# Kernel tuning notes

Measured on AMD Instinct MI355X. Metric: run time of the kernel, lower is better.

The kernel has to match this reference:

```python
import jax, jax.numpy as jnp
import numpy as np

B, T, I, U, O, BB = 256, 1024, 64, 256, 64, 128  # batch, seq, input, units, output, backbone_units

def lecun_tanh(x):
    return 1.7159 * jnp.tanh(0.666 * x)

def setup_inputs() -> dict:
    key = jax.random.key(0)
    ks = jax.random.split(key, 13)
    def lin(k, fan_in, fan_out):
        bound = 1.0 / np.sqrt(fan_in)
        kw, kb = jax.random.split(k)
        W = jax.random.uniform(kw, (fan_in, fan_out), jnp.float32, -bound, bound)
        b = jax.random.uniform(kb, (fan_out,), jnp.float32, -bound, bound)
        return W, b
    x = jax.random.normal(ks[0], (B, T, I), jnp.float32)
    W_bb, b_bb = lin(ks[1], I + U, BB)   # backbone Linear
    W_ff1, b_ff1 = lin(ks[2], BB, U)
    W_ff2, b_ff2 = lin(ks[3], BB, U)
    W_ta, b_ta = lin(ks[4], BB, U)       # time_a
    W_tb, b_tb = lin(ks[5], BB, U)       # time_b
    W_fc, b_fc = lin(ks[6], U, O)        # readout
    return {"x": x, "W_bb": W_bb, "b_bb": b_bb, "W_ff1": W_ff1, "b_ff1": b_ff1,
            "W_ff2": W_ff2, "b_ff2": b_ff2, "W_ta": W_ta, "b_ta": b_ta,
            "W_tb": W_tb, "b_tb": b_tb, "W_fc": W_fc, "b_fc": b_fc}

def reference(x, W_bb, b_bb, W_ff1, b_ff1, W_ff2, b_ff2, W_ta, b_ta, W_tb, b_tb, W_fc, b_fc):
    ts = jnp.float32(1.0)  # default elapsed time per step
    def step(h, xt):
        z = jnp.concatenate([xt, h], axis=-1)          # [B, I+U]
        g = lecun_tanh(z @ W_bb + b_bb)                # [B, BB]
        ff1 = jnp.tanh(g @ W_ff1 + b_ff1)              # [B, U]
        ff2 = jnp.tanh(g @ W_ff2 + b_ff2)
        t_interp = jax.nn.sigmoid((g @ W_ta + b_ta) * ts + (g @ W_tb + b_tb))
        h_new = ff1 * (1.0 - t_interp) + t_interp * ff2
        return h_new, h_new
    h0 = jnp.zeros((x.shape[0], U), x.dtype)
    h_last, hs = jax.lax.scan(step, h0, jnp.swapaxes(x, 0, 1))  # hs: [T, B, U]
    hs = jnp.swapaxes(hs, 0, 1)                                  # [B, T, U]
    out = hs @ W_fc + b_fc                                       # [B, T, O]
    return out, h_last
```

## Files before the change

### kernel.cpp

```cpp
#include <hip/hip_runtime.h>
#include <stdint.h>

#define B_ 256
#define T_ 1024
#define I_ 64
#define U_ 256
#define O_ 64
#define BB_ 128

typedef unsigned int u32;
typedef unsigned short u16;
typedef _Float16 half2_t __attribute__((ext_vector_type(2)));
typedef _Float16 f16x8 __attribute__((ext_vector_type(8)));
typedef float f32x4 __attribute__((ext_vector_type(4)));

#if defined(__has_builtin)
#if __has_builtin(__builtin_amdgcn_fdot2)
#define USE_DOT2 1
#else
#define USE_DOT2 0
#endif
#else
#define USE_DOT2 0
#endif

static __device__ __forceinline__ u32 packpair(float a, float b) {
  half2_t h; h.x = (_Float16)a; h.y = (_Float16)b;
  return __builtin_bit_cast(u32, h);
}
static __device__ __forceinline__ float unpack_lo(u32 u) {
  half2_t h = __builtin_bit_cast(half2_t, u); return (float)h.x;
}
static __device__ __forceinline__ float unpack_hi(u32 u) {
  half2_t h = __builtin_bit_cast(half2_t, u); return (float)h.y;
}
static __device__ __forceinline__ float dot2acc(u32 w, u32 z, float acc) {
#if USE_DOT2
  return __builtin_amdgcn_fdot2(__builtin_bit_cast(half2_t, w),
                                __builtin_bit_cast(half2_t, z), acc, false);
#else
  half2_t hw = __builtin_bit_cast(half2_t, w);
  half2_t hz = __builtin_bit_cast(half2_t, z);
  acc += (float)hw.x * (float)hz.x;
  acc += (float)hw.y * (float)hz.y;
  return acc;
#endif
}

template <int CTRL>
static __device__ __forceinline__ float dpp_mov_f(float v) {
  return __builtin_bit_cast(float, __builtin_amdgcn_update_dpp(
      0, __builtin_bit_cast(int, v), CTRL, 0xF, 0xF, true));
}
#define DPP_XOR1 0xB1
#define DPP_XOR2 0x4E
#define DPP_HMIR 0x141
#define DPP_MIRR 0x140

static __device__ __forceinline__ float fast_tanh(float x) {
  return 1.0f - 2.0f / (1.0f + __expf(2.0f * x));
}
static __device__ __forceinline__ float fast_sigmoid(float x) {
  return 1.0f / (1.0f + __expf(-x));
}

static __device__ __forceinline__ float rcpf(float x) {
#if defined(__has_builtin) && __has_builtin(__builtin_amdgcn_rcpf)
  return __builtin_amdgcn_rcpf(x);
#else
  return 1.0f / x;
#endif
}
static __device__ __forceinline__ float exp2fast(float x) {
#if defined(__has_builtin) && __has_builtin(__builtin_amdgcn_exp2f)
  return __builtin_amdgcn_exp2f(x);
#else
  return exp2f(x);
#endif
}

static __device__ __forceinline__ f32x4 mfma16(uint4 a, uint4 b, f32x4 c) {
  return __builtin_amdgcn_mfma_f32_16x16x32_f16(
      __builtin_bit_cast(f16x8, a), __builtin_bit_cast(f16x8, b), c, 0, 0, 0);
}

#define LOG2E 1.44269504f

__global__ __launch_bounds__(512, 2)
void px_kernel(const float* __restrict__ x,
               const float* __restrict__ W_bb, const float* __restrict__ b_bb,
               u32* __restrict__ Px)
{
  const int tid = threadIdx.x;
  const int l   = tid & 63;
  const int w   = tid >> 6;
  const int c16 = l & 15;
  const int q4  = l >> 4;
  const int rr  = blockIdx.x;
  const int t0  = blockIdx.y * 64;

  uint4 wpx[2];
  {
    const int colb = w * 16 + c16;
#pragma unroll
    for (int c = 0; c < 2; ++c) {
      u32 qv[4];
#pragma unroll
      for (int q = 0; q < 4; ++q) {
        const int k0 = c * 32 + q4 * 8 + 2 * q;
        qv[q] = packpair(W_bb[(size_t)k0 * BB_ + colb],
                         W_bb[(size_t)(k0 + 1) * BB_ + colb]);
      }
      wpx[c] = make_uint4(qv[0], qv[1], qv[2], qv[3]);
    }
  }
  const float bc = b_bb[w * 16 + c16];

  const float* xr = x + ((size_t)(rr * 16 + c16)) * T_ * I_ + q4 * 8;
  uint2* __restrict__ pxo =
      (uint2*)Px + ((size_t)rr * T_ + t0) * 512 + w * 64 + l;

  for (int i = 0; i < 64; ++i) {
    const int t = t0 + i;
    const float* xt = xr + (size_t)t * I_;
    float4 v0 = *(const float4*)(xt);
    float4 v1 = *(const float4*)(xt + 4);
    float4 v2 = *(const float4*)(xt + 32);
    float4 v3 = *(const float4*)(xt + 36);
    uint4 a0 = make_uint4(packpair(v0.x, v0.y), packpair(v0.z, v0.w),
                          packpair(v1.x, v1.y), packpair(v1.z, v1.w));
    uint4 a1 = make_uint4(packpair(v2.x, v2.y), packpair(v2.z, v2.w),
                          packpair(v3.x, v3.y), packpair(v3.z, v3.w));
    f32x4 acc = {bc, bc, bc, bc};
    acc = mfma16(a0, wpx[0], acc);
    acc = mfma16(a1, wpx[1], acc);
    uint2 o;
    o.x = packpair(acc[0], acc[1]);
    o.y = packpair(acc[2], acc[3]);
    pxo[(size_t)i * 512] = o;
  }
}

template <bool PX>
__global__ __launch_bounds__(512, 2)
void cfc_mfma(const float* __restrict__ x,
              const float* __restrict__ W_bb, const float* __restrict__ b_bb,
              const float* __restrict__ W_ff1, const float* __restrict__ b_ff1,
              const float* __restrict__ W_ff2, const float* __restrict__ b_ff2,
              const float* __restrict__ W_ta,  const float* __restrict__ b_ta,
              const float* __restrict__ W_tb,  const float* __restrict__ b_tb,
              float* __restrict__ out, u32* __restrict__ Hbuf,
              const u32* __restrict__ Px)
{
  __shared__ __align__(16) u32 s_z[2560];
  __shared__ __align__(16) u32 s_g[1024];

  const int tid = threadIdx.x;
  const int l   = tid & 63;
  const int w   = tid >> 6;
  const int c16 = l & 15;
  const int q4  = l >> 4;
  const int odd = l & 1;
  const int rr  = blockIdx.x;
  const int row0 = rr * 16;

  const int NBB = PX ? 8 : 10;
  const int KOFF = PX ? 64 : 0;
  uint4 wbb[10];
  {
    const int colb = w * 16 + c16;
    for (int c = 0; c < NBB; ++c) {
      u32 qv[4];
#pragma unroll
      for (int q = 0; q < 4; ++q) {
        const int k0 = KOFF + c * 32 + q4 * 8 + 2 * q;
        qv[q] = packpair(W_bb[(size_t)k0 * BB_ + colb],
                         W_bb[(size_t)(k0 + 1) * BB_ + colb]);
      }
      wbb[c] = make_uint4(qv[0], qv[1], qv[2], qv[3]);
    }
  }
  uint4 wff[3][2][4];
#pragma unroll
  for (int ut = 0; ut < 2; ++ut) {
    const int u = w * 32 + ut * 16 + c16;
#pragma unroll
    for (int c = 0; c < 4; ++c) {
      u32 qa[4], qb[4], qc[4];
#pragma unroll
      for (int q = 0; q < 4; ++q) {
        const int k0 = c * 32 + q4 * 8 + 2 * q;
        const size_t i0 = (size_t)k0 * U_ + u, i1 = i0 + U_;
        qa[q] = packpair(W_ff1[i0], W_ff1[i1]);
        qb[q] = packpair(W_ff2[i0], W_ff2[i1]);
        qc[q] = packpair(W_ta[i0] + W_tb[i0], W_ta[i1] + W_tb[i1]);
      }
      wff[0][ut][c] = make_uint4(qa[0], qa[1], qa[2], qa[3]);
      wff[1][ut][c] = make_uint4(qb[0], qb[1], qb[2], qb[3]);
      wff[2][ut][c] = make_uint4(qc[0], qc[1], qc[2], qc[3]);
    }
  }

  const float bgs = PX ? 0.f : b_bb[w * 16 + c16] * (1.332f * LOG2E);
  float b1s[2], b2s[2], btn[2];
#pragma unroll
  for (int ut = 0; ut < 2; ++ut) {
    const int u = w * 32 + ut * 16 + c16;
    b1s[ut] = b_ff1[u] * (2.0f * LOG2E);
    b2s[ut] = b_ff2[u] * (2.0f * LOG2E);
    btn[ut] = -(b_ta[u] + b_tb[u]) * LOG2E;
  }

  const int mx = tid >> 5, px_ = tid & 31;
  const float* xptr = x + (size_t)(row0 + mx) * T_ * I_ + 2 * px_;
  const int zxw = ((px_ >> 4) * 64 + mx + 16 * ((px_ >> 2) & 3)) * 4 + (px_ & 3);

  const uint2* pxp = (const uint2*)Px + (size_t)rr * T_ * 512 + w * 64 + l;

  const int rbase = odd ? 2 : 0;
  const int m0 = q4 * 4 + rbase, m1 = m0 + 1;
  const int pg = w * 8 + (c16 >> 1);
  const int gw0 = ((pg >> 4) * 64 + 16 * ((pg >> 2) & 3)) * 4 + (pg & 3)
                  + 16 * q4 + (odd ? 8 : 0);
  int zw_[2]; size_t hb0_[2], hb1_[2];
#pragma unroll
  for (int ut = 0; ut < 2; ++ut) {
    const int pu = w * 16 + ut * 8 + (c16 >> 1);
    zw_[ut] = ((2 + (pu >> 4)) * 64 + 16 * ((pu >> 2) & 3)) * 4 + (pu & 3)
              + 16 * q4 + (odd ? 8 : 0);
    hb0_[ut] = (size_t)(row0 + m0) * T_ * 128 + pu;
    hb1_[ut] = (size_t)(row0 + m1) * T_ * 128 + pu;
  }

  reinterpret_cast<uint4*>(s_z)[128 + tid] = make_uint4(0u, 0u, 0u, 0u);
  uint2 pxc;
  if (PX) {
    pxc = pxp[0];
  } else {
    __syncthreads();
    float2 xv = *(const float2*)xptr;
    s_z[zxw] = packpair(xv.x, xv.y);
  }
  __syncthreads();

  const uint4* z4 = (const uint4*)s_z;
  const uint4* g4 = (const uint4*)s_g;

  for (int t = 0; t < T_; ++t) {
    uint2 pxn;
    float2 xv;
    const bool more = (t + 1 < T_);
    if (PX) {
      if (more) pxn = pxp[(size_t)(t + 1) * 512];
    } else {
      if (more) xv = *(const float2*)(xptr + (size_t)(t + 1) * I_);
    }

    f32x4 aA, aB = {0.f, 0.f, 0.f, 0.f};
    if (PX) {
      aA = (f32x4){unpack_lo(pxc.x), unpack_hi(pxc.x),
                   unpack_lo(pxc.y), unpack_hi(pxc.y)};
      aA = mfma16(z4[2 * 64 + l], wbb[0], aA);
      aB = mfma16(z4[3 * 64 + l], wbb[1], aB);
      aA = mfma16(z4[4 * 64 + l], wbb[2], aA);
      aB = mfma16(z4[5 * 64 + l], wbb[3], aB);
      aA = mfma16(z4[6 * 64 + l], wbb[4], aA);
      aB = mfma16(z4[7 * 64 + l], wbb[5], aB);
      aA = mfma16(z4[8 * 64 + l], wbb[6], aA);
      aB = mfma16(z4[9 * 64 + l], wbb[7], aB);
    } else {
      aA = (f32x4){0.f, 0.f, 0.f, 0.f};
#pragma unroll
      for (int c = 0; c < 10; c += 2) {
        aA = mfma16(z4[c * 64 + l],       wbb[c],     aA);
        aB = mfma16(z4[(c + 1) * 64 + l], wbb[c + 1], aB);
      }
    }
    const f32x4 ab = aA + aB;

    u32 gq[4];
#pragma unroll
    for (int r = 0; r < 4; ++r) {
      const float a  = __builtin_fmaf(ab[r], 1.332f * LOG2E, bgs);
      const float rv = rcpf(exp2fast(a) + 1.0f);
      const float g  = __builtin_fmaf(rv, -3.4318f, 1.7159f);
      const float gp = dpp_mov_f<DPP_XOR1>(g);
      gq[r] = odd ? packpair(gp, g) : packpair(g, gp);
    }
    s_g[gw0]     = odd ? gq[2] : gq[0];
    s_g[gw0 + 4] = odd ? gq[3] : gq[1];
    __syncthreads();

    f32x4 af[3][2];
#pragma unroll
    for (int mt = 0; mt < 3; ++mt)
#pragma unroll
      for (int ut = 0; ut < 2; ++ut)
        af[mt][ut] = (f32x4){0.f, 0.f, 0.f, 0.f};
#pragma unroll
    for (int c = 0; c < 4; ++c) {
      const uint4 ga = g4[c * 64 + l];
#pragma unroll
      for (int mt = 0; mt < 3; ++mt)
#pragma unroll
        for (int ut = 0; ut < 2; ++ut)
          af[mt][ut] = mfma16(ga, wff[mt][ut][c], af[mt][ut]);
    }

#pragma unroll
    for (int ut = 0; ut < 2; ++ut) {
      u32 hq[4];
#pragma unroll
      for (int r = 0; r < 4; ++r) {
        const float E1 = exp2fast(__builtin_fmaf(af[0][ut][r], 2.0f * LOG2E, b1s[ut]));
        const float E2 = exp2fast(__builtin_fmaf(af[1][ut][r], 2.0f * LOG2E, b2s[ut]));
        const float E3 = exp2fast(__builtin_fmaf(af[2][ut][r], -LOG2E, btn[ut]));
        const float p2 = E2 + 1.0f, p3 = E3 + 1.0f;
        const float qq = p2 * p3;
        const float D  = __builtin_fmaf(E1, qq, qq);
        const float R  = rcpf(D);
        const float u2 = (E2 - E1) - qq;
        const float h  = __builtin_fmaf(R + R, u2, 1.0f);
        const float hp = dpp_mov_f<DPP_XOR1>(h);
        hq[r] = odd ? packpair(hp, h) : packpair(h, hp);
      }
      const u32 s0 = odd ? hq[2] : hq[0];
      const u32 s1 = odd ? hq[3] : hq[1];
      s_z[zw_[ut]]     = s0;
      s_z[zw_[ut] + 4] = s1;
      Hbuf[hb0_[ut] + (size_t)t * 128] = s0;
      Hbuf[hb1_[ut] + (size_t)t * 128] = s1;
    }
    if (PX) {
      pxc = pxn;
    } else {
      if (more) s_z[zxw] = packpair(xv.x, xv.y);
    }
    __syncthreads();
  }

  {
    const uint4 hv = reinterpret_cast<const uint4*>(s_z)[128 + tid];
    float2* tail = (float2*)(out + (size_t)B_ * T_ * O_);
#pragma unroll
    for (int i = 0; i < 4; ++i) {
      const int vh   = tid * 4 + i;
      const int ch   = vh >> 8;
      const int lane = (vh >> 2) & 63;
      const int slot = vh & 3;
      const int m    = lane & 15;
      const int bq   = lane >> 4;
      const int pu   = ch * 16 + bq * 4 + slot;
      const u32 hp   = (i == 0) ? hv.x : (i == 1) ? hv.y : (i == 2) ? hv.z : hv.w;
      float2 hf; hf.x = unpack_lo(hp); hf.y = unpack_hi(hp);
      tail[(size_t)(row0 + m) * 128 + pu] = hf;
    }
  }
}

template <bool DEFER>
__global__ __launch_bounds__(1024)
void cfc_kernel(const float* __restrict__ x,
                const float* __restrict__ W_bb, const float* __restrict__ b_bb,
                const float* __restrict__ W_ff1, const float* __restrict__ b_ff1,
                const float* __restrict__ W_ff2, const float* __restrict__ b_ff2,
                const float* __restrict__ W_ta,  const float* __restrict__ b_ta,
                const float* __restrict__ W_tb,  const float* __restrict__ b_tb,
                const float* __restrict__ W_fc,  const float* __restrict__ b_fc,
                float* __restrict__ out, u32* __restrict__ Hbuf)
{
  __shared__ __align__(16) u32 s_z2[160];
  __shared__ __align__(16) u32 s_g2[64];
  u16* s_gh = (u16*)s_g2;

  const int tid = threadIdx.x;
  const int r   = blockIdx.x;

  const int ca  = tid >> 3;
  const int kga = tid & 7;
  const int jb = tid >> 2;
  const int kq = tid & 3;
  const int ro = tid >> 4;
  const int rk = tid & 15;

  u32 wbb[20];
#pragma unroll
  for (int j = 0; j < 5; ++j)
#pragma unroll
    for (int q = 0; q < 4; ++q) {
      int p = 4 * (kga + 8 * j) + q;
      wbb[4 * j + q] = packpair(W_bb[(2 * p) * BB_ + ca],
                                W_bb[(2 * p + 1) * BB_ + ca]);
    }
  u32 wf1[16], wf2[16], wta[16], wtb[16];
#pragma unroll
  for (int j = 0; j < 4; ++j)
#pragma unroll
    for (int q = 0; q < 4; ++q) {
      int p = 4 * (kq + 4 * j) + q;
      int k0 = 2 * p, k1 = 2 * p + 1;
      wf1[4 * j + q] = packpair(W_ff1[k0 * U_ + jb], W_ff1[k1 * U_ + jb]);
      wf2[4 * j + q] = packpair(W_ff2[k0 * U_ + jb], W_ff2[k1 * U_ + jb]);
      wta[4 * j + q] = packpair(W_ta [k0 * U_ + jb], W_ta [k1 * U_ + jb]);
      wtb[4 * j + q] = packpair(W_tb [k0 * U_ + jb], W_tb [k1 * U_ + jb]);
    }
  u32 wfc[8];
  float bfo = 0.f;
  if (!DEFER) {
#pragma unroll
    for (int j = 0; j < 2; ++j)
#pragma unroll
      for (int q = 0; q < 4; ++q) {
        int p = 4 * (rk + 16 * j) + q;
        wfc[4 * j + q] = packpair(W_fc[(2 * p) * O_ + ro],
                                  W_fc[(2 * p + 1) * O_ + ro]);
      }
    bfo = b_fc[ro];
  }
  const float bbbc = b_bb[ca];
  const float b1 = b_ff1[jb], b2 = b_ff2[jb];
  const float bta = b_ta[jb], btb = b_tb[jb];

  const float* xrow = x + (size_t)r * T_ * I_;
  const size_t out_row = (size_t)r * T_ * O_;
  u32* __restrict__ hrow = DEFER ? (Hbuf + (size_t)r * T_ * (U_ / 2)) : nullptr;

  if (tid < 160) s_z2[tid] = 0u;
  __syncthreads();
  if (tid < 32) {
    float2 xv = ((const float2*)xrow)[tid];
    s_z2[tid] = packpair(xv.x, xv.y);
  }
  __syncthreads();

  for (int t = 0; t < T_; ++t) {
    float2 xv;
    const bool ldx = (tid < 32) && (t + 1 < T_);
    if (ldx) xv = ((const float2*)(xrow + (size_t)(t + 1) * I_))[tid];

    float bacc = 0.f;
#pragma unroll
    for (int j = 0; j < 5; ++j) {
      uint4 zz = *reinterpret_cast<const uint4*>(s_z2 + 4 * (kga + 8 * j));
      bacc = dot2acc(wbb[4 * j + 0], zz.x, bacc);
      bacc = dot2acc(wbb[4 * j + 1], zz.y, bacc);
      bacc = dot2acc(wbb[4 * j + 2], zz.z, bacc);
      bacc = dot2acc(wbb[4 * j + 3], zz.w, bacc);
    }
    bacc += dpp_mov_f<DPP_XOR1>(bacc);
    bacc += dpp_mov_f<DPP_XOR2>(bacc);
    bacc += dpp_mov_f<DPP_HMIR>(bacc);
    float g = 1.7159f * fast_tanh(0.666f * (bacc + bbbc));

    float racc = 0.f;
    if (!DEFER) {
#pragma unroll
      for (int j = 0; j < 2; ++j) {
        uint4 hh = *reinterpret_cast<const uint4*>(s_z2 + 32 + 4 * (rk + 16 * j));
        racc = dot2acc(wfc[4 * j + 0], hh.x, racc);
        racc = dot2acc(wfc[4 * j + 1], hh.y, racc);
        racc = dot2acc(wfc[4 * j + 2], hh.z, racc);
        racc = dot2acc(wfc[4 * j + 3], hh.w, racc);
      }
      racc += dpp_mov_f<DPP_XOR1>(racc);
      racc += dpp_mov_f<DPP_XOR2>(racc);
      racc += dpp_mov_f<DPP_HMIR>(racc);
      racc += dpp_mov_f<DPP_MIRR>(racc);
    }
    if ((tid & 7) == 0)
      s_gh[ca] = __builtin_bit_cast(u16, (_Float16)g);
    if (!DEFER && t > 0 && rk == 0)
      out[out_row + (size_t)(t - 1) * O_ + ro] = racc + bfo;
    __syncthreads();

    float a1 = 0.f, a2 = 0.f, a3 = 0.f, a4 = 0.f;
#pragma unroll
    for (int j = 0; j < 4; ++j) {
      uint4 gg = *reinterpret_cast<const uint4*>(s_g2 + 4 * (kq + 4 * j));
      a1 = dot2acc(wf1[4 * j + 0], gg.x, a1);
      a1 = dot2acc(wf1[4 * j + 1], gg.y, a1);
      a1 = dot2acc(wf1[4 * j + 2], gg.z, a1);
      a1 = dot2acc(wf1[4 * j + 3], gg.w, a1);
      a2 = dot2acc(wf2[4 * j + 0], gg.x, a2);
      a2 = dot2acc(wf2[4 * j + 1], gg.y, a2);
      a2 = dot2acc(wf2[4 * j + 2], gg.z, a2);
      a2 = dot2acc(wf2[4 * j + 3], gg.w, a2);
      a3 = dot2acc(wta[4 * j + 0], gg.x, a3);
      a3 = dot2acc(wta[4 * j + 1], gg.y, a3);
      a3 = dot2acc(wta[4 * j + 2], gg.z, a3);
      a3 = dot2acc(wta[4 * j + 3], gg.w, a3);
      a4 = dot2acc(wtb[4 * j + 0], gg.x, a4);
      a4 = dot2acc(wtb[4 * j + 1], gg.y, a4);
      a4 = dot2acc(wtb[4 * j + 2], gg.z, a4);
      a4 = dot2acc(wtb[4 * j + 3], gg.w, a4);
    }
    a1 += dpp_mov_f<DPP_XOR1>(a1); a1 += dpp_mov_f<DPP_XOR2>(a1);
    a2 += dpp_mov_f<DPP_XOR1>(a2); a2 += dpp_mov_f<DPP_XOR2>(a2);
    a3 += dpp_mov_f<DPP_XOR1>(a3); a3 += dpp_mov_f<DPP_XOR2>(a3);
    a4 += dpp_mov_f<DPP_XOR1>(a4); a4 += dpp_mov_f<DPP_XOR2>(a4);
    float f1 = fast_tanh(a1 + b1);
    float f2 = fast_tanh(a2 + b2);
    float ti = fast_sigmoid(a3 + bta + a4 + btb);
    float h  = f1 + ti * (f2 - f1);
    float hq = dpp_mov_f<DPP_HMIR>(h);

    if ((tid & 7) == 0) {
      u32 pr = packpair(h, hq);
      int m = tid >> 3;
      s_z2[32 + m] = pr;
      if (DEFER) hrow[(size_t)t * (U_ / 2) + m] = pr;
    }
    if (ldx) s_z2[tid] = packpair(xv.x, xv.y);
    __syncthreads();
  }

  if (!DEFER) {
    float racc = 0.f;
#pragma unroll
    for (int j = 0; j < 2; ++j) {
      uint4 hh = *reinterpret_cast<const uint4*>(s_z2 + 32 + 4 * (rk + 16 * j));
      racc = dot2acc(wfc[4 * j + 0], hh.x, racc);
      racc = dot2acc(wfc[4 * j + 1], hh.y, racc);
      racc = dot2acc(wfc[4 * j + 2], hh.z, racc);
      racc = dot2acc(wfc[4 * j + 3], hh.w, racc);
    }
    racc += dpp_mov_f<DPP_XOR1>(racc);
    racc += dpp_mov_f<DPP_XOR2>(racc);
    racc += dpp_mov_f<DPP_HMIR>(racc);
    racc += dpp_mov_f<DPP_MIRR>(racc);
    if (rk == 0)
      out[out_row + (size_t)(T_ - 1) * O_ + ro] = racc + bfo;
  }

  if (tid < 128) {
    u32 hp = s_z2[32 + tid];
    float2 hv; hv.x = unpack_lo(hp); hv.y = unpack_hi(hp);
    ((float2*)(out + (size_t)B_ * T_ * O_))[r * 128 + tid] = hv;
  }
}

__global__ __launch_bounds__(512)
void ro_kernel(const u32* __restrict__ Hbuf,
               const float* __restrict__ W_fc, const float* __restrict__ b_fc,
               float* __restrict__ out)
{
  __shared__ __align__(16) u32 s_h[8 * 128];
  const int tid = threadIdx.x;
  const int o   = tid & 63;
  const int w   = tid >> 6;
  const int r   = blockIdx.x;

  u32 wfc[128];
#pragma unroll
  for (int p = 0; p < 128; ++p)
    wfc[p] = packpair(W_fc[(2 * p) * O_ + o], W_fc[(2 * p + 1) * O_ + o]);
  const float bo = b_fc[o];

  const u32* hrow = Hbuf + (size_t)r * T_ * 128;
  const size_t out_row = (size_t)r * T_ * O_;

  for (int c = 0; c < T_ / 8; ++c) {
    *(uint2*)(s_h + 2 * tid) =
        *(const uint2*)(hrow + (size_t)c * 1024 + 2 * tid);
    __syncthreads();
    float acc = bo;
    const uint4* h4 = reinterpret_cast<const uint4*>(s_h + w * 128);
#pragma unroll
    for (int i = 0; i < 32; ++i) {
      uint4 hh = h4[i];
      acc = dot2acc(wfc[4 * i + 0], hh.x, acc);
      acc = dot2acc(wfc[4 * i + 1], hh.y, acc);
      acc = dot2acc(wfc[4 * i + 2], hh.z, acc);
      acc = dot2acc(wfc[4 * i + 3], hh.w, acc);
    }
    out[out_row + (size_t)(8 * c + w) * O_ + o] = acc;
    __syncthreads();
  }
}

extern "C" void kernel_launch(void* const* d_in, const int* in_sizes, int n_in,
                              void* d_out, int out_size, void* d_ws, size_t ws_size,
                              hipStream_t stream) {
  const float* x     = (const float*)d_in[0];
  const float* W_bb  = (const float*)d_in[1];
  const float* b_bb  = (const float*)d_in[2];
  const float* W_ff1 = (const float*)d_in[3];
  const float* b_ff1 = (const float*)d_in[4];
  const float* W_ff2 = (const float*)d_in[5];
  const float* b_ff2 = (const float*)d_in[6];
  const float* W_ta  = (const float*)d_in[7];
  const float* b_ta  = (const float*)d_in[8];
  const float* W_tb  = (const float*)d_in[9];
  const float* b_tb  = (const float*)d_in[10];
  const float* W_fc  = (const float*)d_in[11];
  const float* b_fc  = (const float*)d_in[12];
  float* out = (float*)d_out;

  const size_t h_bytes  = (size_t)B_ * T_ * (U_ / 2) * sizeof(u32);
  const size_t px_bytes = (size_t)B_ * T_ * (BB_ / 2) * sizeof(u32);
  if (ws_size >= h_bytes + px_bytes) {
    u32* Hbuf = (u32*)d_ws;
    u32* Px   = (u32*)((char*)d_ws + h_bytes);
    px_kernel<<<dim3(16, T_ / 64), dim3(512), 0, stream>>>(x, W_bb, b_bb, Px);
    cfc_mfma<true><<<dim3(B_ / 16), dim3(512), 0, stream>>>(
        x, W_bb, b_bb, W_ff1, b_ff1, W_ff2, b_ff2,
        W_ta, b_ta, W_tb, b_tb, out, Hbuf, Px);
    ro_kernel<<<dim3(B_), dim3(512), 0, stream>>>(Hbuf, W_fc, b_fc, out);
  } else if (ws_size >= h_bytes) {
    u32* Hbuf = (u32*)d_ws;
    cfc_mfma<false><<<dim3(B_ / 16), dim3(512), 0, stream>>>(
        x, W_bb, b_bb, W_ff1, b_ff1, W_ff2, b_ff2,
        W_ta, b_ta, W_tb, b_tb, out, Hbuf, nullptr);
    ro_kernel<<<dim3(B_), dim3(512), 0, stream>>>(Hbuf, W_fc, b_fc, out);
  } else {
    cfc_kernel<false><<<dim3(B_), dim3(1024), 0, stream>>>(
        x, W_bb, b_bb, W_ff1, b_ff1, W_ff2, b_ff2,
        W_ta, b_ta, W_tb, b_tb, W_fc, b_fc, out, nullptr);
  }
}
```

Measured before the change: 1.851 ms.

## Add restructured recurrent kernel with new h pairing, swizzled LDS, deferred Hbuf stores

Adds a new recurrent kernel in which each lane packs two hidden units 16 apart (u, u+16) directly instead of exchanging neighbours through DPP. It also XOR-swizzles the LDS layout of the h state to avoid bank conflicts and defers the global stores of h by one step so they overlap the next step's MFMA work. The readout kernel gains a matching weight-pairing variant, and the f16 packing switches to the round-toward-zero pack instruction. The intent is to shorten the serial per-timestep critical path; the trade-off is a different h storage order that has to stay consistent across three kernels, plus slightly different rounding.

Result: faster. 1.649 ms (-10.9%).

```diff
diff --git a/kernel.cpp b/kernel.cpp
--- a/kernel.cpp
+++ b/kernel.cpp
@@ -28,6 +28,15 @@
   half2_t h; h.x = (_Float16)a; h.y = (_Float16)b;
   return __builtin_bit_cast(u32, h);
 }
+#if defined(__has_builtin) && __has_builtin(__builtin_amdgcn_cvt_pkrtz)
+static __device__ __forceinline__ u32 pkrtz(float a, float b) {
+  return __builtin_bit_cast(u32, __builtin_amdgcn_cvt_pkrtz(a, b));
+}
+#else
+static __device__ __forceinline__ u32 pkrtz(float a, float b) {
+  return packpair(a, b);
+}
+#endif
 static __device__ __forceinline__ float unpack_lo(u32 u) {
   half2_t h = __builtin_bit_cast(half2_t, u); return (float)h.x;
 }
@@ -127,17 +136,213 @@
     float4 v1 = *(const float4*)(xt + 4);
     float4 v2 = *(const float4*)(xt + 32);
     float4 v3 = *(const float4*)(xt + 36);
-    uint4 a0 = make_uint4(packpair(v0.x, v0.y), packpair(v0.z, v0.w),
-                          packpair(v1.x, v1.y), packpair(v1.z, v1.w));
-    uint4 a1 = make_uint4(packpair(v2.x, v2.y), packpair(v2.z, v2.w),
-                          packpair(v3.x, v3.y), packpair(v3.z, v3.w));
+    uint4 a0 = make_uint4(pkrtz(v0.x, v0.y), pkrtz(v0.z, v0.w),
+                          pkrtz(v1.x, v1.y), pkrtz(v1.z, v1.w));
+    uint4 a1 = make_uint4(pkrtz(v2.x, v2.y), pkrtz(v2.z, v2.w),
+                          pkrtz(v3.x, v3.y), pkrtz(v3.z, v3.w));
     f32x4 acc = {bc, bc, bc, bc};
     acc = mfma16(a0, wpx[0], acc);
     acc = mfma16(a1, wpx[1], acc);
     uint2 o;
-    o.x = packpair(acc[0], acc[1]);
-    o.y = packpair(acc[2], acc[3]);
+    o.x = pkrtz(acc[0], acc[1]);
+    o.y = pkrtz(acc[2], acc[3]);
     pxo[(size_t)i * 512] = o;
+  }
+}
+
+__global__ __launch_bounds__(512, 2)
+void cfc_mfma2(const float* __restrict__ W_bb,
+               const float* __restrict__ W_ff1, const float* __restrict__ b_ff1,
+               const float* __restrict__ W_ff2, const float* __restrict__ b_ff2,
+               const float* __restrict__ W_ta,  const float* __restrict__ b_ta,
+               const float* __restrict__ W_tb,  const float* __restrict__ b_tb,
+               float* __restrict__ out, u32* __restrict__ Hbuf,
+               const u32* __restrict__ Px)
+{
+  __shared__ __align__(16) u32 s_z[2560];
+  __shared__ __align__(16) u32 s_g[1024];
+
+  const int tid = threadIdx.x;
+  const int l   = tid & 63;
+  const int w   = tid >> 6;
+  const int c16 = l & 15;
+  const int q4  = l >> 4;
+  const int odd = l & 1;
+  const int rr  = blockIdx.x;
+  const int row0 = rr * 16;
+  const int lx  = l ^ (l >> 4);
+
+  uint4 wbb[8];
+  {
+    const int colb = w * 16 + c16;
+#pragma unroll
+    for (int c = 0; c < 8; ++c) {
+      u32 qv[4];
+#pragma unroll
+      for (int q = 0; q < 4; ++q) {
+        const int ulo = 32 * c + 4 * q4 + q;
+        qv[q] = packpair(W_bb[(size_t)(64 + ulo) * BB_ + colb],
+                         W_bb[(size_t)(80 + ulo) * BB_ + colb]);
+      }
+      wbb[c] = make_uint4(qv[0], qv[1], qv[2], qv[3]);
+    }
+  }
+  uint4 wff[3][2][4];
+#pragma unroll
+  for (int ut = 0; ut < 2; ++ut) {
+    const int u = w * 32 + ut * 16 + c16;
+#pragma unroll
+    for (int c = 0; c < 4; ++c) {
+      u32 qa[4], qb[4], qc[4];
+#pragma unroll
+      for (int q = 0; q < 4; ++q) {
+        const int k0 = c * 32 + q4 * 8 + 2 * q;
+        const size_t i0 = (size_t)k0 * U_ + u, i1 = i0 + U_;
+        qa[q] = packpair(W_ff1[i0], W_ff1[i1]);
+        qb[q] = packpair(W_ff2[i0], W_ff2[i1]);
+        qc[q] = packpair(W_ta[i0] + W_tb[i0], W_ta[i1] + W_tb[i1]);
+      }
+      wff[0][ut][c] = make_uint4(qa[0], qa[1], qa[2], qa[3]);
+      wff[1][ut][c] = make_uint4(qb[0], qb[1], qb[2], qb[3]);
+      wff[2][ut][c] = make_uint4(qc[0], qc[1], qc[2], qc[3]);
+    }
+  }
+
+  float b1s[2], b2s[2], btn[2];
+#pragma unroll
+  for (int ut = 0; ut < 2; ++ut) {
+    const int u = w * 32 + ut * 16 + c16;
+    b1s[ut] = b_ff1[u] * (2.0f * LOG2E);
+    b2s[ut] = b_ff2[u] * (2.0f * LOG2E);
+    btn[ut] = -(b_ta[u] + b_tb[u]) * LOG2E;
+  }
+
+  const uint2* pxp = (const uint2*)Px + (size_t)rr * T_ * 512 + w * 64 + l;
+
+  const int pg = w * 8 + (c16 >> 1);
+  const int gw0 = ((pg >> 4) * 64 + 16 * ((pg >> 2) & 3)) * 4 + (pg & 3)
+                  + 16 * q4 + (odd ? 8 : 0);
+
+  int zws_[4];
+#pragma unroll
+  for (int r = 0; r < 4; ++r) {
+    const int lane_cons = 4 * q4 + r + 16 * (c16 >> 2);
+    const int LB = (2 + w) * 64 + lane_cons;
+    const int SB = LB ^ (c16 >> 2);
+    zws_[r] = SB * 4 + (c16 & 3);
+  }
+  u32* hp_[4];
+#pragma unroll
+  for (int r = 0; r < 4; ++r)
+    hp_[r] = Hbuf + (size_t)(row0 + 4 * q4 + r) * T_ * 128 + (w * 16 + c16);
+
+  reinterpret_cast<uint4*>(s_z)[128 + tid] = make_uint4(0u, 0u, 0u, 0u);
+  uint2 pxc = pxp[0];
+  __syncthreads();
+
+  const uint4* z4 = (const uint4*)s_z;
+  const uint4* g4 = (const uint4*)s_g;
+
+  u32 hold0 = 0, hold1 = 0, hold2 = 0, hold3 = 0;
+
+  for (int t = 0; t < T_; ++t) {
+    uint2 pxn;
+    const bool more = (t + 1 < T_);
+    if (more) pxn = pxp[(size_t)(t + 1) * 512];
+
+    f32x4 aA = {unpack_lo(pxc.x), unpack_hi(pxc.x),
+                unpack_lo(pxc.y), unpack_hi(pxc.y)};
+    f32x4 aB = {0.f, 0.f, 0.f, 0.f};
+    aA = mfma16(z4[2 * 64 + lx], wbb[0], aA);
+    aB = mfma16(z4[3 * 64 + lx], wbb[1], aB);
+    aA = mfma16(z4[4 * 64 + lx], wbb[2], aA);
+    aB = mfma16(z4[5 * 64 + lx], wbb[3], aB);
+    aA = mfma16(z4[6 * 64 + lx], wbb[4], aA);
+    aB = mfma16(z4[7 * 64 + lx], wbb[5], aB);
+    aA = mfma16(z4[8 * 64 + lx], wbb[6], aA);
+    aB = mfma16(z4[9 * 64 + lx], wbb[7], aB);
+    const f32x4 ab = aA + aB;
+
+    u32 gq[4];
+#pragma unroll
+    for (int r = 0; r < 4; ++r) {
+      const float a  = ab[r] * (1.332f * LOG2E);
+      const float rv = rcpf(exp2fast(a) + 1.0f);
+      const float g  = __builtin_fmaf(rv, -3.4318f, 1.7159f);
+      const float gp = dpp_mov_f<DPP_XOR1>(g);
+      gq[r] = odd ? pkrtz(gp, g) : pkrtz(g, gp);
+    }
+    s_g[gw0]     = odd ? gq[2] : gq[0];
+    s_g[gw0 + 4] = odd ? gq[3] : gq[1];
+    __syncthreads();
+
+    if (t) {
+      const size_t o = (size_t)(t - 1) * 128;
+      hp_[0][o] = hold0; hp_[1][o] = hold1;
+      hp_[2][o] = hold2; hp_[3][o] = hold3;
+    }
+
+    f32x4 af[3][2];
+#pragma unroll
+    for (int mt = 0; mt < 3; ++mt)
+#pragma unroll
+      for (int ut = 0; ut < 2; ++ut)
+        af[mt][ut] = (f32x4){0.f, 0.f, 0.f, 0.f};
+#pragma unroll
+    for (int c = 0; c < 4; ++c) {
+      const uint4 ga = g4[c * 64 + l];
+#pragma unroll
+      for (int mt = 0; mt < 3; ++mt)
+#pragma unroll
+        for (int ut = 0; ut < 2; ++ut)
+          af[mt][ut] = mfma16(ga, wff[mt][ut][c], af[mt][ut]);
+    }
+
+    u32 pk0, pk1, pk2, pk3;
+#pragma unroll
+    for (int r = 0; r < 4; ++r) {
+      float h01[2];
+#pragma unroll
+      for (int ut = 0; ut < 2; ++ut) {
+        const float E1 = exp2fast(__builtin_fmaf(af[0][ut][r], 2.0f * LOG2E, b1s[ut]));
+        const float E2 = exp2fast(__builtin_fmaf(af[1][ut][r], 2.0f * LOG2E, b2s[ut]));
+        const float E3 = exp2fast(__builtin_fmaf(af[2][ut][r], -LOG2E, btn[ut]));
+        const float p2 = E2 + 1.0f, p3 = E3 + 1.0f;
+        const float qq = p2 * p3;
+        const float D  = __builtin_fmaf(E1, qq, qq);
+        const float R  = rcpf(D);
+        const float u2 = (E2 - E1) - qq;
+        h01[ut] = __builtin_fmaf(R + R, u2, 1.0f);
+      }
+      const u32 pkv = pkrtz(h01[0], h01[1]);
+      s_z[zws_[r]] = pkv;
+      if (r == 0) pk0 = pkv; else if (r == 1) pk1 = pkv;
+      else if (r == 2) pk2 = pkv; else pk3 = pkv;
+    }
+    hold0 = pk0; hold1 = pk1; hold2 = pk2; hold3 = pk3;
+    pxc = pxn;
+    __syncthreads();
+  }
+
+  {
+    const size_t o = (size_t)(T_ - 1) * 128;
+    hp_[0][o] = hold0; hp_[1][o] = hold1;
+    hp_[2][o] = hold2; hp_[3][o] = hold3;
+  }
+
+  {
+    const int c  = tid >> 6;
+    const int tl = tid & 63;
+    const uint4 hv = z4[(2 + c) * 64 + (tl ^ (tl >> 4))];
+    const int row = row0 + (tl & 15);
+    const int ub  = 32 * c + 4 * (tl >> 4);
+    float* tail = out + (size_t)B_ * T_ * O_ + (size_t)row * 256;
+#pragma unroll
+    for (int q = 0; q < 4; ++q) {
+      const u32 hp = (q == 0) ? hv.x : (q == 1) ? hv.y : (q == 2) ? hv.z : hv.w;
+      tail[ub + q]      = unpack_lo(hp);
+      tail[ub + q + 16] = unpack_hi(hp);
+    }
   }
 }
 
@@ -250,11 +455,8 @@
     uint2 pxn;
     float2 xv;
     const bool more = (t + 1 < T_);
-    if (PX) {
-      if (more) pxn = pxp[(size_t)(t + 1) * 512];
-    } else {
-      if (more) xv = *(const float2*)(xptr + (size_t)(t + 1) * I_);
-    }
+    if (PX) { if (more) pxn = pxp[(size_t)(t + 1) * 512]; }
+    else    { if (more) xv = *(const float2*)(xptr + (size_t)(t + 1) * I_); }
 
     f32x4 aA, aB = {0.f, 0.f, 0.f, 0.f};
     if (PX) {
@@ -331,11 +533,8 @@
       Hbuf[hb0_[ut] + (size_t)t * 128] = s0;
       Hbuf[hb1_[ut] + (size_t)t * 128] = s1;
     }
-    if (PX) {
-      pxc = pxn;
-    } else {
-      if (more) s_z[zxw] = packpair(xv.x, xv.y);
-    }
+    if (PX) { pxc = pxn; }
+    else    { if (more) s_z[zxw] = packpair(xv.x, xv.y); }
     __syncthreads();
   }
 
@@ -539,6 +738,7 @@
   }
 }
 
+template <bool NEWPAIR>
 __global__ __launch_bounds__(512)
 void ro_kernel(const u32* __restrict__ Hbuf,
                const float* __restrict__ W_fc, const float* __restrict__ b_fc,
@@ -552,8 +752,15 @@
 
   u32 wfc[128];
 #pragma unroll
-  for (int p = 0; p < 128; ++p)
-    wfc[p] = packpair(W_fc[(2 * p) * O_ + o], W_fc[(2 * p + 1) * O_ + o]);
+  for (int p = 0; p < 128; ++p) {
+    if (NEWPAIR) {
+      const int ulo = 32 * (p >> 4) + (p & 15);
+      wfc[p] = packpair(W_fc[(size_t)ulo * O_ + o],
+                        W_fc[(size_t)(ulo + 16) * O_ + o]);
+    } else {
+      wfc[p] = packpair(W_fc[(2 * p) * O_ + o], W_fc[(2 * p + 1) * O_ + o]);
+    }
+  }
   const float bo = b_fc[o];
 
   const u32* hrow = Hbuf + (size_t)r * T_ * 128;
@@ -602,16 +809,16 @@
     u32* Hbuf = (u32*)d_ws;
     u32* Px   = (u32*)((char*)d_ws + h_bytes);
     px_kernel<<<dim3(16, T_ / 64), dim3(512), 0, stream>>>(x, W_bb, b_bb, Px);
-    cfc_mfma<true><<<dim3(B_ / 16), dim3(512), 0, stream>>>(
-        x, W_bb, b_bb, W_ff1, b_ff1, W_ff2, b_ff2,
+    cfc_mfma2<<<dim3(B_ / 16), dim3(512), 0, stream>>>(
+        W_bb, W_ff1, b_ff1, W_ff2, b_ff2,
         W_ta, b_ta, W_tb, b_tb, out, Hbuf, Px);
-    ro_kernel<<<dim3(B_), dim3(512), 0, stream>>>(Hbuf, W_fc, b_fc, out);
+    ro_kernel<true><<<dim3(B_), dim3(512), 0, stream>>>(Hbuf, W_fc, b_fc, out);
   } else if (ws_size >= h_bytes) {
     u32* Hbuf = (u32*)d_ws;
     cfc_mfma<false><<<dim3(B_ / 16), dim3(512), 0, stream>>>(
         x, W_bb, b_bb, W_ff1, b_ff1, W_ff2, b_ff2,
         W_ta, b_ta, W_tb, b_tb, out, Hbuf, nullptr);
-    ro_kernel<<<dim3(B_), dim3(512), 0, stream>>>(Hbuf, W_fc, b_fc, out);
+    ro_kernel<false><<<dim3(B_), dim3(512), 0, stream>>>(Hbuf, W_fc, b_fc, out);
   } else {
     cfc_kernel<false><<<dim3(B_), dim3(1024), 0, stream>>>(
         x, W_bb, b_bb, W_ff1, b_ff1, W_ff2, b_ff2,
```
